# Kernel optimization log

Hardware: AMD Instinct MI355X
Metric: run time of the kernel (lower is better)

Reference implementation:

```python
import jax, jax.numpy as jnp
import numpy as np

NUM_HEADS = 16
D_MODEL = 1024
D_K = D_MODEL // NUM_HEADS


def setup_inputs() -> dict:
    key = jax.random.key(0)
    ks = jax.random.split(key, 11)
    B, S, D = 1, 4096, D_MODEL
    scale = 1.0 / np.sqrt(D)
    return {
        "Q": jax.random.normal(ks[0], (B, S, D), jnp.float32),
        "K": jax.random.normal(ks[1], (B, S, D), jnp.float32),
        "V": jax.random.normal(ks[2], (B, S, D), jnp.float32),
        "W_Q": jax.random.normal(ks[3], (D, D), jnp.float32) * scale,
        "b_Q": jax.random.normal(ks[4], (D,), jnp.float32) * 0.02,
        "W_K": jax.random.normal(ks[5], (D, D), jnp.float32) * scale,
        "b_K": jax.random.normal(ks[6], (D,), jnp.float32) * 0.02,
        "W_V": jax.random.normal(ks[7], (D, D), jnp.float32) * scale,
        "b_V": jax.random.normal(ks[8], (D,), jnp.float32) * 0.02,
        "W_O": jax.random.normal(ks[9], (D, D), jnp.float32) * scale,
        "b_O": jax.random.normal(ks[10], (D,), jnp.float32) * 0.02,
    }


def _split_heads(x):
    # (B, S, D) -> (B, H, S, d_k)
    B, S, _ = x.shape
    return x.reshape(B, S, NUM_HEADS, D_K).transpose(0, 2, 1, 3)


def reference(Q, K, V, W_Q, b_Q, W_K, b_K, W_V, b_V, W_O, b_O):
    q = _split_heads(Q @ W_Q + b_Q)  # (B, H, S, d_k)
    k = _split_heads(K @ W_K + b_K)
    v = _split_heads(V @ W_V + b_V)
    inv_sqrt_dk = jnp.asarray(1.0 / np.sqrt(D_K), q.dtype)
    scores = jnp.einsum("bhqd,bhkd->bhqk", q, k) * inv_sqrt_dk  # (B, H, S, S)
    weights = jax.nn.softmax(scores, axis=-1)
    out = jnp.einsum("bhqk,bhkd->bhqd", weights, v)  # (B, H, S, d_k)
    B, _, S, _ = out.shape
    combined = out.transpose(0, 2, 1, 3).reshape(B, S, D_MODEL)
    return combined @ W_O + b_O
```

## Files before the change

### kernel.cpp

```cpp
#include <hip/hip_runtime.h>

typedef float f32x2 __attribute__((ext_vector_type(2)));
typedef float f32x4 __attribute__((ext_vector_type(4)));
typedef float f32x16 __attribute__((ext_vector_type(16)));
typedef short bf16x8 __attribute__((ext_vector_type(8)));
typedef unsigned u32x2 __attribute__((ext_vector_type(2)));
typedef unsigned short u16;

#define S_LEN 4096
#define DMODEL 1024
#define NH 16
#define DK 64

#define SCALE_Q 0.18033688f

static __device__ __forceinline__ u16 f2bf(float x) {
  union { float f; unsigned u; } v; v.f = x;
  unsigned r = v.u + 0x7fffu + ((v.u >> 16) & 1u);
  return (u16)(r >> 16);
}

static __device__ __forceinline__ float bf2f(u16 x) {
  union { unsigned u; float f; } v; v.u = ((unsigned)x) << 16;
  return v.f;
}

#if __has_builtin(__builtin_amdgcn_exp2f)
#define EXP2F __builtin_amdgcn_exp2f
#else
#define EXP2F exp2f
#endif

static __device__ __forceinline__ unsigned pkbf(float lo, float hi) {
  unsigned r;
  asm("v_cvt_pk_bf16_f32 %0, %1, %2" : "=v"(r) : "v"(lo), "v"(hi));
  return r;
}

static __device__ __forceinline__ void plswap(unsigned& a, unsigned& b, int hi) {
#if __has_builtin(__builtin_amdgcn_permlane32_swap)
  u32x2 r = __builtin_amdgcn_permlane32_swap(a, b, false, false);
  a = r.x; b = r.y;
  (void)hi;
#else
  unsigned ax = __shfl_xor(a, 32), bx = __shfl_xor(b, 32);
  unsigned na = hi ? bx : a;
  unsigned nb = hi ? b : ax;
  a = na; b = nb;
#endif
}

static __device__ __forceinline__ void gload16(const void* g, void* l) {
  void* gg = (void*)g;
  __builtin_amdgcn_global_load_lds(
      (__attribute__((address_space(1))) void*)gg,
      (__attribute__((address_space(3))) void*)l, 16, 0, 0);
}

__global__ __launch_bounds__(256) void wcast_t(const float* __restrict__ W,
                                               u16* __restrict__ Wt) {
  __shared__ float t[32][33];
  const int x = threadIdx.x, y = threadIdx.y;
  const int n0 = blockIdx.x * 32, k0 = blockIdx.y * 32;
#pragma unroll
  for (int i = 0; i < 4; ++i)
    t[y + 8 * i][x] = W[(size_t)(k0 + y + 8 * i) * DMODEL + n0 + x];
  __syncthreads();
#pragma unroll
  for (int i = 0; i < 4; ++i)
    Wt[(size_t)(n0 + y + 8 * i) * DMODEL + k0 + x] = f2bf(t[x][y + 8 * i]);
}

__global__ __launch_bounds__(256) void castbf(const float* __restrict__ in,
                                              u16* __restrict__ out, int n8) {
  int i = blockIdx.x * 256 + threadIdx.x;
  const int stride = gridDim.x * 256;
  for (; i < n8; i += stride) {
    float4 a = ((const float4*)in)[2 * i];
    float4 b = ((const float4*)in)[2 * i + 1];
    union { ushort4 u[2]; int4 q; } t;
    t.u[0].x = f2bf(a.x); t.u[0].y = f2bf(a.y);
    t.u[0].z = f2bf(a.z); t.u[0].w = f2bf(a.w);
    t.u[1].x = f2bf(b.x); t.u[1].y = f2bf(b.y);
    t.u[1].z = f2bf(b.z); t.u[1].w = f2bf(b.w);
    ((int4*)out)[i] = t.q;
  }
}

template <int MODE>
__global__ __launch_bounds__(256) void pgemm(const u16* __restrict__ Abase,
                                             const u16* __restrict__ Btbase,
                                             const float* __restrict__ bq,
                                             const float* __restrict__ bk,
                                             const float* __restrict__ bv,
                                             void* __restrict__ outbase) {
  __shared__ __align__(16) char Al[16384];
  __shared__ __align__(16) char Bl[16384];
  const int nblk = gridDim.x, cpx = nblk >> 3;
  const int b0 = blockIdx.x;
  const int bid = (b0 & 7) * cpx + (b0 >> 3);
  const int z = (MODE == 0) ? (bid >> 8) : 0;
  const int rem = bid & 255;
  const int nb = rem & 7, mb = rem >> 3;
  const int m0 = mb * 128, n0 = nb * 128;
  const int tid = threadIdx.x, lane = tid & 63, wid = tid >> 6;
  const int gq = lane >> 4, c16 = lane & 15;
  const int wm = (wid >> 1) * 64, wn = (wid & 1) * 64;
  const char* Ab = (const char*)(Abase + (size_t)z * S_LEN * DMODEL);
  const char* Bb = (const char*)(Btbase + (size_t)z * DMODEL * DMODEL);
  const float* bias = (z == 0) ? bq : (z == 1 ? bk : bv);
  const float scale = (MODE == 0 && z == 0) ? SCALE_Q : 1.0f;

  f32x4 acc[4][4] = {};

  for (int kt = 0; kt < 16; ++kt) {
    const int kb = kt * 128;
#pragma unroll
    for (int p = 0; p < 4; ++p) {
      int lin = p * 4096 + tid * 16;
      int row = lin >> 7;
      int colg = (lin & 127) ^ ((row & 7) << 4);
      gload16(Ab + (size_t)(m0 + row) * 2048 + kb + colg,
              Al + p * 4096 + wid * 1024);
    }
#pragma unroll
    for (int p = 0; p < 4; ++p) {
      int lin = p * 4096 + tid * 16;
      int row = lin >> 7;
      int colg = (lin & 127) ^ ((row & 7) << 4);
      gload16(Bb + (size_t)(n0 + row) * 2048 + kb + colg,
              Bl + p * 4096 + wid * 1024);
    }
    __syncthreads();
#pragma unroll
    for (int kk = 0; kk < 2; ++kk) {
      bf16x8 a[4], b[4];
#pragma unroll
      for (int m = 0; m < 4; ++m) {
        int row = wm + m * 16 + c16;
        a[m] = *(const bf16x8*)(Al + row * 128 +
                                ((kk * 64 + gq * 16) ^ ((row & 7) << 4)));
      }
#pragma unroll
      for (int n = 0; n < 4; ++n) {
        int row = wn + n * 16 + c16;
        b[n] = *(const bf16x8*)(Bl + row * 128 +
                                ((kk * 64 + gq * 16) ^ ((row & 7) << 4)));
      }
#pragma unroll
      for (int m = 0; m < 4; ++m)
#pragma unroll
        for (int n = 0; n < 4; ++n)
          acc[m][n] =
              __builtin_amdgcn_mfma_f32_16x16x32_bf16(a[m], b[n], acc[m][n], 0, 0, 0);
    }
    __syncthreads();
  }

#pragma unroll
  for (int m = 0; m < 4; ++m) {
#pragma unroll
    for (int n = 0; n < 4; ++n) {
      const int row = m0 + wm + m * 16 + gq * 4;
      const int col = n0 + wn + n * 16 + c16;
      const float bb = bias[col];
      if (MODE == 1) {
        float* of = (float*)outbase;
#pragma unroll
        for (int j = 0; j < 4; ++j)
          of[(size_t)(row + j) * DMODEL + col] = acc[m][n][j] + bb;
      } else if (z == 2) {
        u16* ov = (u16*)outbase + (size_t)2 * S_LEN * DMODEL;
        ushort4 u;
        u.x = f2bf(acc[m][n][0] + bb);
        u.y = f2bf(acc[m][n][1] + bb);
        u.z = f2bf(acc[m][n][2] + bb);
        u.w = f2bf(acc[m][n][3] + bb);
        *(ushort4*)(ov + ((size_t)(col >> 6) * DK + (col & 63)) * S_LEN + row) = u;
      } else {
        u16* oq = (u16*)outbase + (size_t)z * S_LEN * DMODEL;
#pragma unroll
        for (int j = 0; j < 4; ++j)
          oq[((size_t)(col >> 6) * S_LEN + row + j) * DK + (col & 63)] =
              f2bf((acc[m][n][j] + bb) * scale);
      }
    }
  }
}

__global__ __launch_bounds__(512) void attn2(const u16* __restrict__ q,
                                             const u16* __restrict__ k,
                                             const u16* __restrict__ vt,
                                             u16* __restrict__ Opart,
                                             float* __restrict__ Lpart) {
  __shared__ __align__(16) char smem[32768];
  const int bid0 = blockIdx.x;
  const int bid = (bid0 & 7) * 64 + (bid0 >> 3);
  const int h = bid >> 5;
  const int kvh = (bid >> 4) & 1;
  const int qblk = bid & 15;
  const int tid = threadIdx.x;
  const int wid = tid >> 6, lane = tid & 63;
  const int l31 = lane & 31, hi = lane >> 5;

  const char* kpb = (const char*)k + (size_t)h * S_LEN * (DK * 2);
  const char* vtb = (const char*)vt + (size_t)h * DK * (S_LEN * 2);

  const int q0w = qblk * 256 + wid * 32;
  const u16* qrow = q + ((size_t)h * S_LEN + q0w + l31) * DK;
  bf16x8 qf[4];
#pragma unroll
  for (int dt = 0; dt < 4; ++dt)
    qf[dt] = *(const bf16x8*)(qrow + dt * 16 + hi * 8);

  f32x16 o0 = {}, o1 = {};
  f32x2 lacc2 = {0.f, 0.f};

  const int woff = wid << 10;
  const int kt0 = kvh * 32;
  const int kt1 = kt0 + 32;

  const int swz = (l31 & 7) << 4;
  int dsa[4];
#pragma unroll
  for (int dt = 0; dt < 4; ++dt)
    dsa[dt] = (l31 << 7) + ((dt * 32 + hi * 16) ^ swz);

  const int lin = tid * 16;
  const int sw = lin ^ (((lin >> 7) & 7) << 4);
  const char* gk = kpb + (size_t)kt0 * 8192 + sw;
  const char* gv = vtb + (size_t)(lin >> 7) * 8192 + (size_t)kt0 * 128 + (sw & 127);

  gload16(gk, smem + woff);          gk += 8192;
  gload16(gv, smem + 8192 + woff);   gv += 128;
  __syncthreads();

  auto body = [&](const int CUR, const int NXT, bool doStage) {
    if (doStage) {
      gload16(gk, smem + NXT + woff);          gk += 8192;
      gload16(gv, smem + NXT + 8192 + woff);   gv += 128;
    }
    const char* kb = smem + CUR;
    const char* vb = smem + CUR + 8192;

    f32x16 st0 = {}, st1 = {};
    __builtin_amdgcn_s_setprio(1);
#pragma unroll
    for (int dt = 0; dt < 4; ++dt) {
      bf16x8 k0 = *(const bf16x8*)(kb + dsa[dt]);
      bf16x8 k1 = *(const bf16x8*)(kb + 4096 + dsa[dt]);
      st0 = __builtin_amdgcn_mfma_f32_32x32x16_bf16(k0, qf[dt], st0, 0, 0, 0);
      st1 = __builtin_amdgcn_mfma_f32_32x32x16_bf16(k1, qf[dt], st1, 0, 0, 0);
    }
    __builtin_amdgcn_s_setprio(0);

    unsigned w0[8], w1[8];
    f32x2 s2 = {0.f, 0.f};
#pragma unroll
    for (int i = 0; i < 8; ++i) {
      float a0 = EXP2F(st0[2 * i]), a1 = EXP2F(st0[2 * i + 1]);
      f32x2 t = {a0, a1}; s2 += t;
      w0[i] = pkbf(a0, a1);
    }
#pragma unroll
    for (int i = 0; i < 8; ++i) {
      float a0 = EXP2F(st1[2 * i]), a1 = EXP2F(st1[2 * i + 1]);
      f32x2 t = {a0, a1}; s2 += t;
      w1[i] = pkbf(a0, a1);
    }
    lacc2 += s2;

    union UF { unsigned w[4]; bf16x8 v; };
    UF f[4];
#pragma unroll
    for (int g = 0; g < 2; ++g) {
#pragma unroll
      for (int j = 0; j < 2; ++j) {
        unsigned a = w0[4 * g + j], b = w0[4 * g + j + 2];
        plswap(a, b, hi);
        f[g].w[j] = a; f[g].w[j + 2] = b;
        unsigned c = w1[4 * g + j], d = w1[4 * g + j + 2];
        plswap(c, d, hi);
        f[2 + g].w[j] = c; f[2 + g].w[j + 2] = d;
      }
    }

    __builtin_amdgcn_s_setprio(1);
#pragma unroll
    for (int kt2 = 0; kt2 < 4; ++kt2) {
      bf16x8 v0 = *(const bf16x8*)(vb + dsa[kt2]);
      bf16x8 v1 = *(const bf16x8*)(vb + 4096 + dsa[kt2]);
      o0 = __builtin_amdgcn_mfma_f32_32x32x16_bf16(v0, f[kt2].v, o0, 0, 0, 0);
      o1 = __builtin_amdgcn_mfma_f32_32x32x16_bf16(v1, f[kt2].v, o1, 0, 0, 0);
    }
    __builtin_amdgcn_s_setprio(0);

    __syncthreads();
  };

  for (int kt = kt0; kt < kt1; kt += 2) {
    body(0, 16384, kt + 1 < kt1);
    body(16384, 0, kt + 2 < kt1);
  }

  const float lacc = lacc2.x + lacc2.y;
  const float lrow = lacc + __shfl_xor(lacc, 32);
  u16* Ob = Opart + ((((size_t)kvh * NH + h) * S_LEN) + q0w + l31) * DK;
#pragma unroll
  for (int g = 0; g < 4; ++g) {
    ushort4 u0, u1;
    u0.x = f2bf(o0[g * 4 + 0]); u0.y = f2bf(o0[g * 4 + 1]);
    u0.z = f2bf(o0[g * 4 + 2]); u0.w = f2bf(o0[g * 4 + 3]);
    *(ushort4*)(Ob + 8 * g + 4 * hi) = u0;
    u1.x = f2bf(o1[g * 4 + 0]); u1.y = f2bf(o1[g * 4 + 1]);
    u1.z = f2bf(o1[g * 4 + 2]); u1.w = f2bf(o1[g * 4 + 3]);
    *(ushort4*)(Ob + 32 + 8 * g + 4 * hi) = u1;
  }
  Lpart[((size_t)kvh * NH + h) * S_LEN + q0w + l31] = lrow;
}

__global__ __launch_bounds__(256) void combine(const u16* __restrict__ Op,
                                               const float* __restrict__ Lp,
                                               u16* __restrict__ comb) {
  const int id = blockIdx.x * 256 + threadIdx.x;
  const int h = id >> 16;
  const int rem = id & 65535;
  const int qv = rem >> 4;
  const int d4 = (rem & 15) << 2;
  const size_t str = (size_t)NH * S_LEN * DK;
  const size_t base = (((size_t)h * S_LEN) + qv) * DK + d4;
  float o0 = 0.f, o1 = 0.f, o2 = 0.f, o3 = 0.f, l = 0.f;
#pragma unroll
  for (int kv = 0; kv < 2; ++kv) {
    ushort4 u = *(const ushort4*)(Op + kv * str + base);
    o0 += bf2f(u.x); o1 += bf2f(u.y); o2 += bf2f(u.z); o3 += bf2f(u.w);
    l += Lp[(size_t)kv * NH * S_LEN + (size_t)h * S_LEN + qv];
  }
  const float inv = 1.f / l;
  ushort4 u;
  u.x = f2bf(o0 * inv);
  u.y = f2bf(o1 * inv);
  u.z = f2bf(o2 * inv);
  u.w = f2bf(o3 * inv);
  *(ushort4*)(comb + (size_t)qv * DMODEL + h * DK + d4) = u;
}

extern "C" void kernel_launch(void* const* d_in, const int* in_sizes, int n_in,
                              void* d_out, int out_size, void* d_ws, size_t ws_size,
                              hipStream_t stream) {
  (void)in_sizes; (void)n_in; (void)out_size; (void)ws_size;
  const float* Q   = (const float*)d_in[0];
  const float* K   = (const float*)d_in[1];
  const float* V   = (const float*)d_in[2];
  const float* W_Q = (const float*)d_in[3];
  const float* b_Q = (const float*)d_in[4];
  const float* W_K = (const float*)d_in[5];
  const float* b_K = (const float*)d_in[6];
  const float* W_V = (const float*)d_in[7];
  const float* b_V = (const float*)d_in[8];
  const float* W_O = (const float*)d_in[9];
  const float* b_O = (const float*)d_in[10];
  float* out = (float*)d_out;

  char* ws = (char*)d_ws;
  const size_t MB = 1024 * 1024;
  u16* WtQ = (u16*)ws;
  u16* Qbf = (u16*)(ws + 8 * MB);
  u16* Opart = (u16*)(ws + 8 * MB);
  u16* qp   = (u16*)(ws + 40 * MB);
  u16* kp   = qp + (size_t)S_LEN * DMODEL;
  u16* vtp  = kp + (size_t)S_LEN * DMODEL;
  u16* comb = vtp + (size_t)S_LEN * DMODEL;
  float* Lpart = (float*)(ws + 72 * MB);

  dim3 tb(32, 8);
  dim3 tg(32, 32);
  wcast_t<<<tg, tb, 0, stream>>>(W_Q, WtQ);
  wcast_t<<<tg, tb, 0, stream>>>(W_K, WtQ + (size_t)DMODEL * DMODEL);
  wcast_t<<<tg, tb, 0, stream>>>(W_V, WtQ + (size_t)2 * DMODEL * DMODEL);
  wcast_t<<<tg, tb, 0, stream>>>(W_O, WtQ + (size_t)3 * DMODEL * DMODEL);

  const int n8 = S_LEN * DMODEL / 8;
  castbf<<<2048, 256, 0, stream>>>(Q, Qbf, n8);
  castbf<<<2048, 256, 0, stream>>>(K, Qbf + (size_t)S_LEN * DMODEL, n8);
  castbf<<<2048, 256, 0, stream>>>(V, Qbf + (size_t)2 * S_LEN * DMODEL, n8);

  pgemm<0><<<768, 256, 0, stream>>>(Qbf, WtQ, b_Q, b_K, b_V, qp);

  attn2<<<512, 512, 0, stream>>>(qp, kp, vtp, Opart, Lpart);
  combine<<<4096, 256, 0, stream>>>(Opart, Lpart, comb);

  pgemm<1><<<256, 256, 0, stream>>>(comb, WtQ + (size_t)3 * DMODEL * DMODEL,
                                    b_O, b_O, b_O, out);
}
```

Before: 177.5 us.

## Batch cast kernels into single launches and relax attention prefetch sync

Merges the four weight transpose-cast launches into one 3D-grid launch and the three input cast launches into one, which removes per-launch overhead and tail gaps between small kernels. In the attention kernel, the full __syncthreads after each tile is replaced with explicit vmcnt waits plus raw s_barrier, so the next tile's async global-to-LDS loads stay in flight while the current tile is computed. This relies on a manual vmcnt count that must match the number of outstanding loads, and could race if that count is wrong.

```diff
diff --git a/kernel.cpp b/kernel.cpp
--- a/kernel.cpp
+++ b/kernel.cpp
@@ -57,9 +57,15 @@
       (__attribute__((address_space(3))) void*)l, 16, 0, 0);
 }
 
-__global__ __launch_bounds__(256) void wcast_t(const float* __restrict__ W,
-                                               u16* __restrict__ Wt) {
+__global__ __launch_bounds__(256) void wcast4(const float* __restrict__ W0,
+                                              const float* __restrict__ W1,
+                                              const float* __restrict__ W2,
+                                              const float* __restrict__ W3,
+                                              u16* __restrict__ Wt) {
   __shared__ float t[32][33];
+  const int z = blockIdx.z;
+  const float* W = (z == 0) ? W0 : (z == 1) ? W1 : (z == 2) ? W2 : W3;
+  u16* dst = Wt + (size_t)z * DMODEL * DMODEL;
   const int x = threadIdx.x, y = threadIdx.y;
   const int n0 = blockIdx.x * 32, k0 = blockIdx.y * 32;
 #pragma unroll
@@ -68,22 +74,27 @@
   __syncthreads();
 #pragma unroll
   for (int i = 0; i < 4; ++i)
-    Wt[(size_t)(n0 + y + 8 * i) * DMODEL + k0 + x] = f2bf(t[x][y + 8 * i]);
-}
-
-__global__ __launch_bounds__(256) void castbf(const float* __restrict__ in,
-                                              u16* __restrict__ out, int n8) {
-  int i = blockIdx.x * 256 + threadIdx.x;
-  const int stride = gridDim.x * 256;
-  for (; i < n8; i += stride) {
-    float4 a = ((const float4*)in)[2 * i];
-    float4 b = ((const float4*)in)[2 * i + 1];
+    dst[(size_t)(n0 + y + 8 * i) * DMODEL + k0 + x] = f2bf(t[x][y + 8 * i]);
+}
+
+__global__ __launch_bounds__(256) void castbf3(const float* __restrict__ A,
+                                               const float* __restrict__ B,
+                                               const float* __restrict__ C,
+                                               u16* __restrict__ out) {
+  const int z = blockIdx.x >> 10;
+  const int b = blockIdx.x & 1023;
+  const float* src = (z == 0) ? A : (z == 1) ? B : C;
+  u16* dst = out + (size_t)z * S_LEN * DMODEL;
+  const int n8 = S_LEN * DMODEL / 8;
+  for (int i = b * 256 + threadIdx.x; i < n8; i += 1024 * 256) {
+    float4 a = ((const float4*)src)[2 * i];
+    float4 c = ((const float4*)src)[2 * i + 1];
     union { ushort4 u[2]; int4 q; } t;
     t.u[0].x = f2bf(a.x); t.u[0].y = f2bf(a.y);
     t.u[0].z = f2bf(a.z); t.u[0].w = f2bf(a.w);
-    t.u[1].x = f2bf(b.x); t.u[1].y = f2bf(b.y);
-    t.u[1].z = f2bf(b.z); t.u[1].w = f2bf(b.w);
-    ((int4*)out)[i] = t.q;
+    t.u[1].x = f2bf(c.x); t.u[1].y = f2bf(c.y);
+    t.u[1].z = f2bf(c.z); t.u[1].w = f2bf(c.w);
+    ((int4*)dst)[i] = t.q;
   }
 }
 
@@ -233,13 +244,17 @@
 
   gload16(gk, smem + woff);          gk += 8192;
   gload16(gv, smem + 8192 + woff);   gv += 128;
-  __syncthreads();
 
   auto body = [&](const int CUR, const int NXT, bool doStage) {
     if (doStage) {
       gload16(gk, smem + NXT + woff);          gk += 8192;
       gload16(gv, smem + NXT + 8192 + woff);   gv += 128;
-    }
+      asm volatile("s_waitcnt vmcnt(2)" ::: "memory");
+    } else {
+      asm volatile("s_waitcnt vmcnt(0)" ::: "memory");
+    }
+    __builtin_amdgcn_s_barrier();
+
     const char* kb = smem + CUR;
     const char* vb = smem + CUR + 8192;
 
@@ -295,7 +310,7 @@
     }
     __builtin_amdgcn_s_setprio(0);
 
-    __syncthreads();
+    __builtin_amdgcn_s_barrier();
   };
 
   for (int kt = kt0; kt < kt1; kt += 2) {
@@ -374,16 +389,10 @@
   float* Lpart = (float*)(ws + 72 * MB);
 
   dim3 tb(32, 8);
-  dim3 tg(32, 32);
-  wcast_t<<<tg, tb, 0, stream>>>(W_Q, WtQ);
-  wcast_t<<<tg, tb, 0, stream>>>(W_K, WtQ + (size_t)DMODEL * DMODEL);
-  wcast_t<<<tg, tb, 0, stream>>>(W_V, WtQ + (size_t)2 * DMODEL * DMODEL);
-  wcast_t<<<tg, tb, 0, stream>>>(W_O, WtQ + (size_t)3 * DMODEL * DMODEL);
-
-  const int n8 = S_LEN * DMODEL / 8;
-  castbf<<<2048, 256, 0, stream>>>(Q, Qbf, n8);
-  castbf<<<2048, 256, 0, stream>>>(K, Qbf + (size_t)S_LEN * DMODEL, n8);
-  castbf<<<2048, 256, 0, stream>>>(V, Qbf + (size_t)2 * S_LEN * DMODEL, n8);
+  dim3 tg4(32, 32, 4);
+  wcast4<<<tg4, tb, 0, stream>>>(W_Q, W_K, W_V, W_O, WtQ);
+
+  castbf3<<<3072, 256, 0, stream>>>(Q, K, V, Qbf);
 
   pgemm<0><<<768, 256, 0, stream>>>(Qbf, WtQ, b_Q, b_K, b_V, qp);
 
```

Measured after the change: 168.7 us. 4.9% less time.
